# Performance work log

Measured on AMD Instinct MI355X. Metric: run time of the kernel, lower is better.

Reference implementation:

```python
import jax, jax.numpy as jnp
import numpy as np

STATE_DIM = 32
ACTION_DIM = 8
LATENT_DIM = 64
HIDDEN = 128
X_DIM = ACTION_DIM + 1  # t channel + actions
B = 4096
L = 128
N_SUB = 2  # fixed RK4 substeps per knot interval


def natural_cubic_coeffs(x):
    """Natural cubic spline on unit-spaced knots 0..L-1 (matches torchcde's
    implicit arange grid). x: [B, L, C]. Returns per-interval coeffs b, c, d
    ([B, L-1, C]) s.t. X(i+u) = x_i + b u + c u^2 + d u^3."""
    Bb, Ln, C = x.shape
    n = Ln - 2
    # tridiagonal system for interior second derivatives (natural BC: m0=mL-1=0)
    M = 4.0 * jnp.eye(n, dtype=x.dtype) + jnp.eye(n, k=1, dtype=x.dtype) + jnp.eye(n, k=-1, dtype=x.dtype)
    rhs = 6.0 * (x[:, 2:] - 2.0 * x[:, 1:-1] + x[:, :-2])  # [B, n, C]
    m_in = jnp.linalg.solve(M, rhs.transpose(1, 0, 2).reshape(n, -1))  # [n, B*C]
    m_in = m_in.reshape(n, Bb, C).transpose(1, 0, 2)
    zpad = jnp.zeros((Bb, 1, C), x.dtype)
    m = jnp.concatenate([zpad, m_in, zpad], axis=1)  # [B, L, C]
    b = (x[:, 1:] - x[:, :-1]) - (2.0 * m[:, :-1] + m[:, 1:]) / 6.0
    c = m[:, :-1] / 2.0
    d = (m[:, 1:] - m[:, :-1]) / 6.0
    return b, c, d


def setup_inputs() -> dict:
    key = jax.random.key(0)
    ks = jax.random.split(key, 8)
    s = jax.random.normal(ks[0], (B, L, STATE_DIM), dtype=jnp.float32)
    a = jax.random.normal(ks[1], (B, L, ACTION_DIM), dtype=jnp.float32)
    t = jnp.broadcast_to(jnp.arange(L, dtype=jnp.float32), (B, L)) + jnp.zeros((B, L), jnp.float32)

    def lin(k, fi, fo, scale=1.0):
        return (jax.random.normal(k, (fi, fo), dtype=jnp.float32) * (scale / np.sqrt(fi))).astype(jnp.float32)

    enc_W = lin(ks[2], STATE_DIM + ACTION_DIM + 1, LATENT_DIM)
    enc_b = jnp.zeros((LATENT_DIM,), jnp.float32)
    f_W1 = lin(ks[3], LATENT_DIM, HIDDEN, 0.5)
    f_b1 = jnp.zeros((HIDDEN,), jnp.float32)
    f_W2 = lin(ks[4], HIDDEN, LATENT_DIM * X_DIM, 0.1)  # small scale keeps the CDE stable over 127 time units
    f_b2 = jnp.zeros((LATENT_DIM * X_DIM,), jnp.float32)
    dec_W = lin(ks[5], LATENT_DIM, STATE_DIM)
    dec_b = jnp.zeros((STATE_DIM,), jnp.float32)
    return dict(s=s, a=a, t=t, enc_W=enc_W, enc_b=enc_b, f_W1=f_W1, f_b1=f_b1,
                f_W2=f_W2, f_b2=f_b2, dec_W=dec_W, dec_b=dec_b)


def reference(s, a, t, enc_W, enc_b, f_W1, f_b1, f_W2, f_b2, dec_W, dec_b):
    # control path X = [t, a] : [B, L, X_DIM]
    x = jnp.concatenate([t[..., None], a], axis=-1)
    cb, cc, cd = natural_cubic_coeffs(x)  # each [B, L-1, X_DIM]

    z0 = jnp.concatenate([s[:, 0], a[:, 0], t[:, 0:1]], axis=-1) @ enc_W + enc_b  # [B, latent]

    def vf(z):  # f(z): [B, latent] -> [B, latent, X_DIM]
        h = jax.nn.relu(z @ f_W1 + f_b1)
        return (h @ f_W2 + f_b2).reshape(-1, LATENT_DIM, X_DIM)

    hstep = 1.0 / N_SUB

    def interval(z, coef):
        bi, ci, di = coef  # [B, X_DIM] each, current interval spline coeffs

        def dzdu(z, u):
            dX = bi + 2.0 * ci * u + 3.0 * di * (u * u)  # dX/dt on this interval
            return jnp.einsum('blx,bx->bl', vf(z), dX)

        for k in range(N_SUB):  # small fixed unroll, not a data-dim loop
            u = k * hstep
            k1 = dzdu(z, u)
            k2 = dzdu(z + 0.5 * hstep * k1, u + 0.5 * hstep)
            k3 = dzdu(z + 0.5 * hstep * k2, u + 0.5 * hstep)
            k4 = dzdu(z + hstep * k3, u + hstep)
            z = z + (hstep / 6.0) * (k1 + 2.0 * k2 + 2.0 * k3 + k4)
        return z, z

    coefs = (cb.transpose(1, 0, 2), cc.transpose(1, 0, 2), cd.transpose(1, 0, 2))  # [L-1, B, X_DIM]
    _, zs = jax.lax.scan(interval, z0, coefs)  # zs: [L-1, B, latent]
    z = jnp.concatenate([z0[None], zs], axis=0).transpose(1, 0, 2)  # [B, L, latent]
    return z @ dec_W + dec_b  # [B, L, state_dim]
```

## Files before the change

### kernel.cpp

```cpp
#include <hip/hip_runtime.h>

#define Bsz 4096
#define Lsz 128
#define NI  127
#define SD  32
#define AD  8
#define LAT 64
#define HID 128
#define BT  16
#define THR 1024

__global__ __launch_bounds__(256) void repack_w2(const float* __restrict__ W2,
                                                 float* __restrict__ W2p8,
                                                 float* __restrict__ W2c0){
  int idx = blockIdx.x*256 + threadIdx.x;
  if (idx < HID*LAT*8){
    int x = idx & 7; int jl = idx >> 3; int l = jl & 63; int j = jl >> 6;
    W2p8[idx] = W2[(j*LAT + l)*9 + x + 1];
  } else if (idx < HID*LAT*9){
    int jl = idx - HID*LAT*8;
    W2c0[jl] = W2[(size_t)jl*9];
  }
}

__global__ __launch_bounds__(256) void spline_kernel(const float* __restrict__ a,
                                                     float* __restrict__ m_ws){
  __shared__ float cp_s[126];
  if (threadIdx.x == 0){
    float c = 0.25f; cp_s[0] = c;
    for (int i=1;i<126;i++){ c = 1.0f/(4.0f - c); cp_s[i] = c; }
  }
  __syncthreads();
  int tid = blockIdx.x*256 + threadIdx.x;
  int b = tid >> 3, c8 = tid & 7;
  float dp[126];
  const float* ab = a + (size_t)b*Lsz*AD + c8;
  float x0 = ab[0];
  float x1 = ab[AD];
  for (int i=0;i<126;i++){
    float x2 = ab[(size_t)(i+2)*AD];
    float rhs = 6.0f*(x2 - 2.0f*x1 + x0);
    dp[i] = (i==0)? rhs*0.25f : (rhs - dp[i-1])*cp_s[i];
    x0 = x1; x1 = x2;
  }
  m_ws[tid] = 0.0f;
  m_ws[((size_t)127*Bsz)*8 + tid] = 0.0f;
  float mn = 0.0f;
  for (int k=125;k>=0;k--){
    mn = dp[k] - cp_s[k]*mn;
    m_ws[((size_t)(k+1)*Bsz)*8 + tid] = mn;
  }
}

#define DPP_XOR1(v) __int_as_float(__builtin_amdgcn_mov_dpp(__float_as_int(v), 0xB1, 0xF, 0xF, true))
#define DPP_XOR2(v) __int_as_float(__builtin_amdgcn_mov_dpp(__float_as_int(v), 0x4E, 0xF, 0xF, true))
#define SWZ_XOR4(v) __int_as_float(__builtin_amdgcn_ds_swizzle(__float_as_int(v), 0x101F))
#define SWZ_XOR8(v) __int_as_float(__builtin_amdgcn_ds_swizzle(__float_as_int(v), 0x201F))

#define HROW 196

__attribute__((amdgpu_waves_per_eu(4,4)))
__global__ __launch_bounds__(THR) void cde_integrate(
    const float* __restrict__ s, const float* __restrict__ a, const float* __restrict__ t,
    const float* __restrict__ encW, const float* __restrict__ encb,
    const float* __restrict__ W1, const float* __restrict__ b1,
    const float* __restrict__ b2, const float* __restrict__ decW, const float* __restrict__ decb,
    const float* __restrict__ W2p8, const float* __restrict__ W2c0, const float* __restrict__ m_ws,
    float* __restrict__ out)
{
  __shared__ float W1t[HID][LAT+4];
  __shared__ float hs[BT][HROW];
  __shared__ float zs[BT][LAT+4];
  __shared__ float dXs[5][BT][8];
  __shared__ float dWs[LAT][SD];
  __shared__ float dbs[SD];

  const int tid = threadIdx.x;
  const int b0 = blockIdx.x * BT;

  for (int i=tid;i<HID*LAT;i+=THR){ int j = i & (HID-1); int k = i >> 7; W1t[j][k] = W1[k*HID+j]; }
  for (int i=tid;i<LAT*SD;i+=THR)  ((float*)dWs)[i] = decW[i];
  if (tid < SD) dbs[tid] = decb[tid];

  const int ol = tid >> 4;
  const int jg = tid & 15;

  float4 wa[8], wb[8]; float wc0[8];
  {
    #pragma unroll
    for (int jj=0;jj<8;jj++){
      const int j = jg*8 + jj;
      const float4* p = (const float4*)&W2p8[((size_t)j*LAT + ol)*8];
      wa[jj] = p[0]; wb[jj] = p[1];
      wc0[jj] = W2c0[j*LAT + ol];
    }
  }
  float4 b2a, b2b; float b2c0;
  {
    const float* bp = b2 + ol*9;
    b2c0 = bp[0];
    b2a.x = bp[1]; b2a.y = bp[2]; b2a.z = bp[3]; b2a.w = bp[4];
    b2b.x = bp[5]; b2b.y = bp[6]; b2b.z = bp[7]; b2b.w = bp[8];
  }
  const float b1r0 = b1[2*ol], b1r1 = b1[2*ol+1];

  {
    const int bb = tid >> 6;
    const int li = tid & 63;
    const float* sb = s + (size_t)(b0+bb)*Lsz*SD;
    const float* ab = a + (size_t)(b0+bb)*Lsz*AD;
    const float tv = t[(size_t)(b0+bb)*Lsz];
    float acc = encb[li];
    #pragma unroll
    for (int k=0;k<SD;k++) acc = fmaf(sb[k], encW[k*LAT+li], acc);
    #pragma unroll
    for (int k=0;k<AD;k++) acc = fmaf(ab[k], encW[(SD+k)*LAT+li], acc);
    acc = fmaf(tv, encW[(SD+AD)*LAT+li], acc);
    zs[bb][li] = acc;
  }
  __syncthreads();

  if (tid < BT*SD){
    const int bb = tid >> 5; const int o = tid & 31;
    float acc = dbs[o];
    #pragma unroll 8
    for (int k=0;k<LAT;k++) acc = fmaf(zs[bb][k], dWs[k][o], acc);
    out[((size_t)(b0+bb)*Lsz + 0)*SD + o] = acc;
  }

  float zb = zs[jg][ol];
  float ka = 0.f;

  for (int iv=0; iv<NI; iv++){
    if (tid < 5*BT*8){
      int ui = tid >> 7; int r = tid & 127; int bb = r >> 3; int x8 = r & 7;
      float u = 0.25f*(float)ui;
      int gb = b0+bb;
      float m0 = m_ws[((size_t)iv    *Bsz + gb)*8 + x8];
      float m1 = m_ws[((size_t)(iv+1)*Bsz + gb)*8 + x8];
      float xd = a[((size_t)gb*Lsz + iv+1)*AD + x8] - a[((size_t)gb*Lsz + iv)*AD + x8];
      float cb = xd - (2.f*m0 + m1)*(1.f/6.f);
      float cc = 0.5f*m0;
      float cd = (m1 - m0)*(1.f/6.f);
      dXs[ui][bb][x8] = cb + (2.f*cc)*u + (3.f*cd)*(u*u);
    }

    for (int st=0; st<8; st++){
      const int ui = (st+1)>>1;
      const int mode = st & 3;
      __syncthreads();

      {
        const int j0 = 2*ol;
        float acc0 = b1r0, acc1 = b1r1;
        const float4* z4 = (const float4*)&zs[jg][0];
        const float4* w0 = (const float4*)&W1t[j0][0];
        const float4* w1 = (const float4*)&W1t[j0+1][0];
        #pragma unroll
        for (int k4=0;k4<LAT/4;k4++){
          float4 zv = z4[k4]; float4 u0 = w0[k4]; float4 u1 = w1[k4];
          acc0 = fmaf(zv.x,u0.x,acc0); acc0 = fmaf(zv.y,u0.y,acc0);
          acc0 = fmaf(zv.z,u0.z,acc0); acc0 = fmaf(zv.w,u0.w,acc0);
          acc1 = fmaf(zv.x,u1.x,acc1); acc1 = fmaf(zv.y,u1.y,acc1);
          acc1 = fmaf(zv.z,u1.z,acc1); acc1 = fmaf(zv.w,u1.w,acc1);
        }
        float2 hv; hv.x = fmaxf(acc0,0.f); hv.y = fmaxf(acc1,0.f);
        *(float2*)&hs[jg][(j0>>3)*12 + (j0&7)] = hv;
      }
      __syncthreads();

      #pragma unroll
      for (int jj=0;jj<8;jj++){
        asm volatile("" : "+v"(wa[jj].x), "+v"(wa[jj].y), "+v"(wa[jj].z), "+v"(wa[jj].w),
                          "+v"(wb[jj].x), "+v"(wb[jj].y), "+v"(wb[jj].z), "+v"(wb[jj].w),
                          "+v"(wc0[jj]));
      }

      auto gemm2_batch = [&](const int bb0)->float {
        float dz[8];
        #pragma unroll
        for (int i=0;i<8;i++){
          const int b = bb0 + i;
          const float4 dxa = *(const float4*)&dXs[ui][b][0];
          const float4 dxb = *(const float4*)&dXs[ui][b][4];
          const float4 h0 = *(const float4*)&hs[b][jg*12];
          const float4 h1 = *(const float4*)&hs[b][jg*12+4];
          float acc = 0.f;
          #define STEP(JJ, HV) { \
            float wd = fmaf(wa[JJ].x,dxa.x, fmaf(wa[JJ].y,dxa.y, fmaf(wa[JJ].z,dxa.z, fmaf(wa[JJ].w,dxa.w, \
                       fmaf(wb[JJ].x,dxb.x, fmaf(wb[JJ].y,dxb.y, fmaf(wb[JJ].z,dxb.z, fmaf(wb[JJ].w,dxb.w, \
                       wc0[JJ])))))))); \
            acc = fmaf(HV, wd, acc); }
          STEP(0,h0.x) STEP(1,h0.y) STEP(2,h0.z) STEP(3,h0.w)
          STEP(4,h1.x) STEP(5,h1.y) STEP(6,h1.z) STEP(7,h1.w)
          #undef STEP
          dz[i] = acc;
        }
        const bool g1 = (jg&1);
        float nd[4];
        #pragma unroll
        for (int i=0;i<4;i++){
          float lo = dz[2*i], hi = dz[2*i+1];
          float send = g1 ? lo : hi;
          float recv = DPP_XOR1(send);
          float keep = g1 ? hi : lo;
          nd[i] = keep + recv;
        }
        const bool g2 = (jg&2);
        float md[2];
        #pragma unroll
        for (int i=0;i<2;i++){
          float lo = nd[2*i], hi = nd[2*i+1];
          float send = g2 ? lo : hi;
          float recv = DPP_XOR2(send);
          float keep = g2 ? hi : lo;
          md[i] = keep + recv;
        }
        const bool g4 = (jg&4);
        float lo = md[0], hi = md[1];
        float send = g4 ? lo : hi;
        float recv = SWZ_XOR4(send);
        float keep = g4 ? hi : lo;
        float r = keep + recv;
        return r + SWZ_XOR8(r);
      };
      const float totA = gemm2_batch(0);
      const float totB = gemm2_batch(8);

      float bias;
      {
        const float4 dja = *(const float4*)&dXs[ui][jg][0];
        const float4 djb = *(const float4*)&dXs[ui][jg][4];
        bias = fmaf(b2a.x,dja.x, fmaf(b2a.y,dja.y, fmaf(b2a.z,dja.z, fmaf(b2a.w,dja.w,
               fmaf(b2b.x,djb.x, fmaf(b2b.y,djb.y, fmaf(b2b.z,djb.z, fmaf(b2b.w,djb.w, b2c0))))))));
      }
      float dzm = ((jg&8)? totB : totA) + bias;

      if (mode == 0){        ka = dzm;
        zs[jg][ol] = zb + 0.25f*dzm;
      } else if (mode == 1){ ka = fmaf(2.f, dzm, ka);
        zs[jg][ol] = zb + 0.25f*dzm;
      } else if (mode == 2){ ka = fmaf(2.f, dzm, ka);
        zs[jg][ol] = zb + 0.5f*dzm;
      } else {               ka += dzm;
        zb = fmaf(0.5f/6.f, ka, zb);
        zs[jg][ol] = zb;
      }
    }

    __syncthreads();
    if (tid < BT*SD){
      const int bb = tid >> 5; const int o = tid & 31;
      float acc = dbs[o];
      #pragma unroll 8
      for (int k=0;k<LAT;k++) acc = fmaf(zs[bb][k], dWs[k][o], acc);
      out[((size_t)(b0+bb)*Lsz + (iv+1))*SD + o] = acc;
    }
  }
}

extern "C" void kernel_launch(void* const* d_in, const int* in_sizes, int n_in,
                              void* d_out, int out_size, void* d_ws, size_t ws_size,
                              hipStream_t stream){
  const float* s    = (const float*)d_in[0];
  const float* a    = (const float*)d_in[1];
  const float* t    = (const float*)d_in[2];
  const float* encW = (const float*)d_in[3];
  const float* encb = (const float*)d_in[4];
  const float* W1   = (const float*)d_in[5];
  const float* b1   = (const float*)d_in[6];
  const float* W2   = (const float*)d_in[7];
  const float* b2   = (const float*)d_in[8];
  const float* decW = (const float*)d_in[9];
  const float* decb = (const float*)d_in[10];
  float* out = (float*)d_out;
  float* ws  = (float*)d_ws;
  float* W2p8 = ws;
  float* W2c0 = ws + HID*LAT*8;
  float* m_ws = ws + HID*LAT*9;

  hipLaunchKernelGGL(repack_w2, dim3((HID*LAT*9+255)/256), dim3(256), 0, stream, W2, W2p8, W2c0);
  hipLaunchKernelGGL(spline_kernel, dim3(Bsz*8/256), dim3(256), 0, stream, a, m_ws);
  hipLaunchKernelGGL(cde_integrate, dim3(Bsz/BT), dim3(THR), 0, stream,
                     s,a,t,encW,encb,W1,b1,b2,decW,decb,W2p8,W2c0,m_ws,out);
}
```

Baseline: 8.287 ms.

## Pack batch pairs into LDS layout and use v_pk_fma_f32 for second GEMM

Rearranges the hidden activations and dX values in shared memory so two batch rows are interleaved, then computes the W2·dX·h contraction with packed two-wide FP32 FMA instructions. The cross-lane reduction is restructured to operate on pairs, with one final DPP exchange. Biases move from registers to shared memory to free VGPRs. The change aims to halve VALU instruction count in the inner loop, at the cost of inline asm and different LDS access patterns, with possible bank conflicts.

```diff
diff --git a/kernel.cpp b/kernel.cpp
--- a/kernel.cpp
+++ b/kernel.cpp
@@ -9,6 +9,9 @@
 #define HID 128
 #define BT  16
 #define THR 1024
+
+typedef float f32x2 __attribute__((ext_vector_type(2)));
+typedef float f32x4 __attribute__((ext_vector_type(4)));
 
 __global__ __launch_bounds__(256) void repack_w2(const float* __restrict__ W2,
                                                  float* __restrict__ W2p8,
@@ -57,7 +60,17 @@
 #define SWZ_XOR4(v) __int_as_float(__builtin_amdgcn_ds_swizzle(__float_as_int(v), 0x101F))
 #define SWZ_XOR8(v) __int_as_float(__builtin_amdgcn_ds_swizzle(__float_as_int(v), 0x201F))
 
-#define HROW 196
+#define PK_MUL_BCLO(d, w, x) asm("v_pk_mul_f32 %0, %1, %2 op_sel:[0,0] op_sel_hi:[0,1]" : "=v"(d) : "v"(w), "v"(x))
+#define PK_FMA_BCLO(acc, w, x) asm("v_pk_fma_f32 %0, %1, %2, %0 op_sel:[0,0,0] op_sel_hi:[0,1,1]" : "+v"(acc) : "v"(w), "v"(x))
+#define PK_FMA_BCHI(acc, w, x) asm("v_pk_fma_f32 %0, %1, %2, %0 op_sel:[1,0,0] op_sel_hi:[1,1,1]" : "+v"(acc) : "v"(w), "v"(x))
+#define PK_FMA(acc, a, b)      asm("v_pk_fma_f32 %0, %1, %2, %0" : "+v"(acc) : "v"(a), "v"(b))
+#define PK_ADD(d, a, b)        asm("v_pk_add_f32 %0, %1, %2" : "=v"(d) : "v"(a), "v"(b))
+
+#define LO2(v4) __builtin_shufflevector(v4, v4, 0, 1)
+#define HI2(v4) __builtin_shufflevector(v4, v4, 2, 3)
+
+#define HPROW 324
+#define DXROW 20
 
 __attribute__((amdgpu_waves_per_eu(4,4)))
 __global__ __launch_bounds__(THR) void cde_integrate(
@@ -69,10 +82,12 @@
     float* __restrict__ out)
 {
   __shared__ float W1t[HID][LAT+4];
-  __shared__ float hs[BT][HROW];
+  __shared__ float hp[8*HPROW];
   __shared__ float zs[BT][LAT+4];
-  __shared__ float dXs[5][BT][8];
+  __shared__ float dXp[5*160];
   __shared__ float dWs[LAT][SD];
+  __shared__ float b1s[HID];
+  __shared__ float b2s[LAT][12];
   __shared__ float dbs[SD];
 
   const int tid = threadIdx.x;
@@ -80,29 +95,27 @@
 
   for (int i=tid;i<HID*LAT;i+=THR){ int j = i & (HID-1); int k = i >> 7; W1t[j][k] = W1[k*HID+j]; }
   for (int i=tid;i<LAT*SD;i+=THR)  ((float*)dWs)[i] = decW[i];
+  if (tid < HID) b1s[tid] = b1[tid];
+  for (int i=tid;i<LAT*12;i+=THR){ int l=i/12, x=i%12; b2s[l][x] = (x<9)? b2[l*9+x] : 0.f; }
   if (tid < SD) dbs[tid] = decb[tid];
 
   const int ol = tid >> 4;
   const int jg = tid & 15;
 
-  float4 wa[8], wb[8]; float wc0[8];
+  f32x2 wpk[8][4]; f32x2 wc0pk[4];
   {
     #pragma unroll
     for (int jj=0;jj<8;jj++){
-      const int j = jg*8 + jj;
-      const float4* p = (const float4*)&W2p8[((size_t)j*LAT + ol)*8];
-      wa[jj] = p[0]; wb[jj] = p[1];
-      wc0[jj] = W2c0[j*LAT + ol];
-    }
-  }
-  float4 b2a, b2b; float b2c0;
-  {
-    const float* bp = b2 + ol*9;
-    b2c0 = bp[0];
-    b2a.x = bp[1]; b2a.y = bp[2]; b2a.z = bp[3]; b2a.w = bp[4];
-    b2b.x = bp[5]; b2b.y = bp[6]; b2b.z = bp[7]; b2b.w = bp[8];
-  }
-  const float b1r0 = b1[2*ol], b1r1 = b1[2*ol+1];
+      const f32x2* p2 = (const f32x2*)&W2p8[((size_t)(jg*8+jj)*LAT + ol)*8];
+      wpk[jj][0]=p2[0]; wpk[jj][1]=p2[1]; wpk[jj][2]=p2[2]; wpk[jj][3]=p2[3];
+    }
+    #pragma unroll
+    for (int q=0;q<4;q++){
+      wc0pk[q].x = W2c0[(jg*8+2*q)*LAT + ol];
+      wc0pk[q].y = W2c0[(jg*8+2*q+1)*LAT + ol];
+    }
+  }
+  const f32x2 one11 = {1.0f, 1.0f};
 
   {
     const int bb = tid >> 6;
@@ -131,6 +144,8 @@
   float zb = zs[jg][ol];
   float ka = 0.f;
 
+  const int hwaddr = (jg>>1)*HPROW + (ol>>2)*20 + ((2*ol)&7)*2 + (jg&1);
+
   for (int iv=0; iv<NI; iv++){
     if (tid < 5*BT*8){
       int ui = tid >> 7; int r = tid & 127; int bb = r >> 3; int x8 = r & 7;
@@ -142,7 +157,7 @@
       float cb = xd - (2.f*m0 + m1)*(1.f/6.f);
       float cc = 0.5f*m0;
       float cd = (m1 - m0)*(1.f/6.f);
-      dXs[ui][bb][x8] = cb + (2.f*cc)*u + (3.f*cd)*(u*u);
+      dXp[ui*160 + (bb>>1)*DXROW + x8*2 + (bb&1)] = cb + (2.f*cc)*u + (3.f*cd)*(u*u);
     }
 
     for (int st=0; st<8; st++){
@@ -152,7 +167,7 @@
 
       {
         const int j0 = 2*ol;
-        float acc0 = b1r0, acc1 = b1r1;
+        float acc0 = b1s[j0], acc1 = b1s[j0+1];
         const float4* z4 = (const float4*)&zs[jg][0];
         const float4* w0 = (const float4*)&W1t[j0][0];
         const float4* w1 = (const float4*)&W1t[j0+1][0];
@@ -164,77 +179,84 @@
           acc1 = fmaf(zv.x,u1.x,acc1); acc1 = fmaf(zv.y,u1.y,acc1);
           acc1 = fmaf(zv.z,u1.z,acc1); acc1 = fmaf(zv.w,u1.w,acc1);
         }
-        float2 hv; hv.x = fmaxf(acc0,0.f); hv.y = fmaxf(acc1,0.f);
-        *(float2*)&hs[jg][(j0>>3)*12 + (j0&7)] = hv;
+        hp[hwaddr]   = fmaxf(acc0, 0.f);
+        hp[hwaddr+2] = fmaxf(acc1, 0.f);
       }
       __syncthreads();
 
+      f32x2 tot0, tot1;
       #pragma unroll
-      for (int jj=0;jj<8;jj++){
-        asm volatile("" : "+v"(wa[jj].x), "+v"(wa[jj].y), "+v"(wa[jj].z), "+v"(wa[jj].w),
-                          "+v"(wb[jj].x), "+v"(wb[jj].y), "+v"(wb[jj].z), "+v"(wb[jj].w),
-                          "+v"(wc0[jj]));
-      }
-
-      auto gemm2_batch = [&](const int bb0)->float {
-        float dz[8];
+      for (int bbat=0; bbat<2; bbat++){
+        f32x2 dzp[4];
         #pragma unroll
-        for (int i=0;i<8;i++){
-          const int b = bb0 + i;
-          const float4 dxa = *(const float4*)&dXs[ui][b][0];
-          const float4 dxb = *(const float4*)&dXs[ui][b][4];
-          const float4 h0 = *(const float4*)&hs[b][jg*12];
-          const float4 h1 = *(const float4*)&hs[b][jg*12+4];
-          float acc = 0.f;
-          #define STEP(JJ, HV) { \
-            float wd = fmaf(wa[JJ].x,dxa.x, fmaf(wa[JJ].y,dxa.y, fmaf(wa[JJ].z,dxa.z, fmaf(wa[JJ].w,dxa.w, \
-                       fmaf(wb[JJ].x,dxb.x, fmaf(wb[JJ].y,dxb.y, fmaf(wb[JJ].z,dxb.z, fmaf(wb[JJ].w,dxb.w, \
-                       wc0[JJ])))))))); \
-            acc = fmaf(HV, wd, acc); }
-          STEP(0,h0.x) STEP(1,h0.y) STEP(2,h0.z) STEP(3,h0.w)
-          STEP(4,h1.x) STEP(5,h1.y) STEP(6,h1.z) STEP(7,h1.w)
-          #undef STEP
-          dz[i] = acc;
+        for (int i=0;i<4;i++){ dzp[i].x = 0.f; dzp[i].y = 0.f; }
+        #pragma unroll
+        for (int pi=0; pi<4; pi++){
+          const int p = bbat*4 + pi;
+          const f32x4* dxq = (const f32x4*)&dXp[ui*160 + p*DXROW];
+          const f32x4* hq  = (const f32x4*)&hp[p*HPROW + jg*20];
+          f32x4 d0=dxq[0], d1=dxq[1], d2=dxq[2], d3=dxq[3];
+          f32x4 g0=hq[0],  g1=hq[1],  g2=hq[2],  g3=hq[3];
+          f32x2 dx2[8] = {LO2(d0),HI2(d0),LO2(d1),HI2(d1),LO2(d2),HI2(d2),LO2(d3),HI2(d3)};
+          f32x2 hh [8] = {LO2(g0),HI2(g0),LO2(g1),HI2(g1),LO2(g2),HI2(g2),LO2(g3),HI2(g3)};
+          #pragma unroll
+          for (int jj=0;jj<8;jj++){
+            f32x2 wd;
+            PK_MUL_BCLO(wd, wpk[jj][0], dx2[0]);
+            PK_FMA_BCHI(wd, wpk[jj][0], dx2[1]);
+            PK_FMA_BCLO(wd, wpk[jj][1], dx2[2]);
+            PK_FMA_BCHI(wd, wpk[jj][1], dx2[3]);
+            PK_FMA_BCLO(wd, wpk[jj][2], dx2[4]);
+            PK_FMA_BCHI(wd, wpk[jj][2], dx2[5]);
+            PK_FMA_BCLO(wd, wpk[jj][3], dx2[6]);
+            PK_FMA_BCHI(wd, wpk[jj][3], dx2[7]);
+            if ((jj&1)==0){ PK_FMA_BCLO(wd, wc0pk[jj>>1], one11); }
+            else          { PK_FMA_BCHI(wd, wc0pk[jj>>1], one11); }
+            PK_FMA(dzp[pi], hh[jj], wd);
+          }
         }
-        const bool g1 = (jg&1);
-        float nd[4];
-        #pragma unroll
-        for (int i=0;i<4;i++){
-          float lo = dz[2*i], hi = dz[2*i+1];
-          float send = g1 ? lo : hi;
-          float recv = DPP_XOR1(send);
-          float keep = g1 ? hi : lo;
-          nd[i] = keep + recv;
-        }
-        const bool g2 = (jg&2);
-        float md[2];
+        const bool g1 = (jg>>1)&1;
+        f32x2 nd[2];
         #pragma unroll
         for (int i=0;i<2;i++){
-          float lo = nd[2*i], hi = nd[2*i+1];
-          float send = g2 ? lo : hi;
-          float recv = DPP_XOR2(send);
-          float keep = g2 ? hi : lo;
-          md[i] = keep + recv;
+          f32x2 lo = dzp[2*i], hi = dzp[2*i+1];
+          f32x2 send = g1 ? lo : hi;
+          f32x2 recv; recv.x = DPP_XOR2(send.x); recv.y = DPP_XOR2(send.y);
+          f32x2 keep = g1 ? hi : lo;
+          PK_ADD(nd[i], keep, recv);
         }
-        const bool g4 = (jg&4);
-        float lo = md[0], hi = md[1];
-        float send = g4 ? lo : hi;
-        float recv = SWZ_XOR4(send);
-        float keep = g4 ? hi : lo;
-        float r = keep + recv;
-        return r + SWZ_XOR8(r);
-      };
-      const float totA = gemm2_batch(0);
-      const float totB = gemm2_batch(8);
-
-      float bias;
+        const bool g2 = (jg>>2)&1;
+        f32x2 md;
+        {
+          f32x2 lo = nd[0], hi = nd[1];
+          f32x2 send = g2 ? lo : hi;
+          f32x2 recv; recv.x = SWZ_XOR4(send.x); recv.y = SWZ_XOR4(send.y);
+          f32x2 keep = g2 ? hi : lo;
+          PK_ADD(md, keep, recv);
+        }
+        f32x2 r8; r8.x = SWZ_XOR8(md.x); r8.y = SWZ_XOR8(md.y);
+        f32x2 totv; PK_ADD(totv, md, r8);
+        if (bbat==0) tot0 = totv; else tot1 = totv;
+      }
+      f32x2 sel = (jg&8) ? tot1 : tot0;
+      float own = (jg&1) ? sel.y : sel.x;
+      float oth = (jg&1) ? sel.x : sel.y;
+      float dzm = own + DPP_XOR1(oth);
+
       {
-        const float4 dja = *(const float4*)&dXs[ui][jg][0];
-        const float4 djb = *(const float4*)&dXs[ui][jg][4];
-        bias = fmaf(b2a.x,dja.x, fmaf(b2a.y,dja.y, fmaf(b2a.z,dja.z, fmaf(b2a.w,dja.w,
-               fmaf(b2b.x,djb.x, fmaf(b2b.y,djb.y, fmaf(b2b.z,djb.z, fmaf(b2b.w,djb.w, b2c0))))))));
+        const f32x4* dxb = (const f32x4*)&dXp[ui*160 + (jg>>1)*DXROW];
+        f32x4 q0=dxb[0], q1=dxb[1], q2=dxb[2], q3=dxb[3];
+        const bool hi = (jg&1);
+        float d0 = hi? q0.y:q0.x, d1 = hi? q0.w:q0.z;
+        float d2 = hi? q1.y:q1.x, d3 = hi? q1.w:q1.z;
+        float d4 = hi? q2.y:q2.x, d5 = hi? q2.w:q2.z;
+        float d6 = hi? q3.y:q3.x, d7 = hi? q3.w:q3.z;
+        const float4 ba = *(const float4*)&b2s[ol][0];
+        const float4 bb4 = *(const float4*)&b2s[ol][4];
+        float bias = fmaf(ba.y,d0, fmaf(ba.z,d1, fmaf(ba.w,d2, fmaf(bb4.x,d3,
+                     fmaf(bb4.y,d4, fmaf(bb4.z,d5, fmaf(bb4.w,d6, fmaf(b2s[ol][8],d7, ba.x))))))));
+        dzm += bias;
       }
-      float dzm = ((jg&8)? totB : totA) + bias;
 
       if (mode == 0){        ka = dzm;
         zs[jg][ol] = zb + 0.25f*dzm;
```

Measured after the change: 8.841 ms. +6.7%, slower.
